# Optimization experiments

Measured on AMD Instinct MI355X. Metric: run time of the kernel, lower is better.

Reference implementation:

```python
import jax, jax.numpy as jnp
import numpy as np

N_HEADS = 16
D_HEAD = 64
D_MODEL = 1024
WINDOW = 256
B, T = 4, 2048


def rotate_half(x):
    x1, x2 = jnp.split(x, 2, axis=-1)
    return jnp.concatenate([-x2, x1], axis=-1)


def apply_rope(x, cos, sin):
    return x * cos + rotate_half(x) * sin


def setup_inputs() -> dict:
    key = jax.random.key(0)
    ks = jax.random.split(key, 5)
    x = jax.random.normal(ks[0], (B, T, D_MODEL), dtype=jnp.float32)
    cos = jax.random.normal(ks[1], (1, T, 1, D_HEAD), dtype=jnp.float32)
    sin = jax.random.normal(ks[2], (1, T, 1, D_HEAD), dtype=jnp.float32)
    qkv_w = jax.random.normal(ks[3], (3 * D_MODEL, D_MODEL), dtype=jnp.float32) * (D_MODEL ** -0.5)
    out_w = jax.random.normal(ks[4], (D_MODEL, D_MODEL), dtype=jnp.float32) * (D_MODEL ** -0.5)
    return {"x": x, "cos": cos, "sin": sin, "qkv_w": qkv_w, "out_w": out_w}


def reference(x, cos, sin, qkv_w, out_w):
    Bc, Tc, C = x.shape
    # QKV projection (bias-free Linear: y = x @ W^T)
    qkv = jnp.einsum('btc,fc->btf', x, qkv_w)
    q, k, v = jnp.split(qkv, 3, axis=-1)
    # [B, H, T, d]
    def to_heads(t):
        return t.reshape(Bc, Tc, N_HEADS, D_HEAD).transpose(0, 2, 1, 3)
    q, k, v = to_heads(q), to_heads(k), to_heads(v)
    # RoPE: cos/sin [1, T, 1, d] -> [1, 1, T, d] broadcasting over heads
    cos_t = cos[:, :Tc].transpose(0, 2, 1, 3)
    sin_t = sin[:, :Tc].transpose(0, 2, 1, 3)
    q = apply_rope(q, cos_t, sin_t)
    k = apply_rope(k, cos_t, sin_t)
    # banded causal mask: allow j <= i and j >= i - (window-1)
    i = jnp.arange(Tc)[:, None]
    j = jnp.arange(Tc)[None, :]
    allowed = (j <= i) & (j >= i - (WINDOW - 1))  # [T, T]
    scale = 1.0 / jnp.sqrt(jnp.asarray(D_HEAD, dtype=q.dtype))
    scores = jnp.einsum('bhqd,bhkd->bhqk', q, k) * scale
    scores = jnp.where(allowed[None, None], scores, jnp.finfo(scores.dtype).min)
    attn = jax.nn.softmax(scores, axis=-1)
    out = jnp.einsum('bhqk,bhkd->bhqd', attn, v)
    out = out.transpose(0, 2, 1, 3).reshape(Bc, Tc, C)
    return jnp.einsum('btc,oc->bto', out, out_w)
```

## Files before the change

kernel.cpp:

```cpp
#include <hip/hip_runtime.h>

typedef __bf16 bf16_t;
typedef __bf16 bf16x8 __attribute__((ext_vector_type(8)));
typedef __bf16 bf16x4 __attribute__((ext_vector_type(4)));
typedef float f32x4 __attribute__((ext_vector_type(4)));

#define GLOAD_LDS16(gptr, lptr)                                                              \
  __builtin_amdgcn_global_load_lds((const __attribute__((address_space(1))) void*)(gptr),    \
                                   (__attribute__((address_space(3))) void*)(lptr), 16, 0, 0)

__device__ __forceinline__ f32x4 f32x4_zero() {
  f32x4 v; v[0] = 0.f; v[1] = 0.f; v[2] = 0.f; v[3] = 0.f; return v;
}

__global__ void cast3_kernel(const float* __restrict__ a, const float* __restrict__ b,
                             const float* __restrict__ c, bf16_t* __restrict__ oa,
                             bf16_t* __restrict__ ob, bf16_t* __restrict__ oc) {
  int i = blockIdx.x * blockDim.x + threadIdx.x;
  const float* src; bf16_t* dst; int j;
  if (i < 2097152) { src = a; dst = oa; j = i; }
  else if (i < 2883584) { src = b; dst = ob; j = i - 2097152; }
  else { src = c; dst = oc; j = i - 2883584; }
  float4 v = ((const float4*)src)[j];
  bf16x4 o;
  o[0] = (bf16_t)v.x; o[1] = (bf16_t)v.y; o[2] = (bf16_t)v.z; o[3] = (bf16_t)v.w;
  ((bf16x4*)dst)[j] = o;
}

template <int MODE>
__global__ __launch_bounds__(256) void gemm_bt_kernel(
    const bf16_t* __restrict__ A, const bf16_t* __restrict__ B, float* __restrict__ C,
    bf16_t* __restrict__ oq, bf16_t* __restrict__ ok_, bf16_t* __restrict__ ov,
    int M, int N, int K) {
  constexpr int BM = 128, BN = 128, BK = 32;
  __shared__ bf16_t As[BM * BK];
  __shared__ bf16_t Bs[BN * BK];
  const int tid = threadIdx.x;
  const int lane = tid & 63;
  const int wid = tid >> 6;
  const int wm = (wid >> 1) * 64;
  const int wn = (wid & 1) * 64;
  const int l16 = lane & 15;
  const int qd = lane >> 4;
  const int bm = blockIdx.x, bn = blockIdx.y;

  const int srow = tid >> 2;
  const int skol = (tid & 3) * 8;

  const bf16_t* gA = A + (size_t)(bm * BM + srow) * K + skol;
  const bf16_t* gB = B + (size_t)(bn * BN + srow) * K + skol;
  bf16_t* lA = &As[srow * BK + skol];
  bf16_t* lB = &Bs[srow * BK + skol];

  f32x4 acc[4][4];
#pragma unroll
  for (int mb = 0; mb < 4; mb++)
#pragma unroll
    for (int nb = 0; nb < 4; nb++) acc[mb][nb] = f32x4_zero();

  for (int k0 = 0; k0 < K; k0 += BK) {
    __syncthreads();
    GLOAD_LDS16(gA + k0, lA);
    GLOAD_LDS16(gA + (size_t)64 * K + k0, lA + 64 * BK);
    GLOAD_LDS16(gB + k0, lB);
    GLOAD_LDS16(gB + (size_t)64 * K + k0, lB + 64 * BK);
    __syncthreads();

    bf16x8 af[4], bfr[4];
#pragma unroll
    for (int mb = 0; mb < 4; mb++)
      af[mb] = *(const bf16x8*)&As[(wm + mb * 16 + l16) * BK + qd * 8];
#pragma unroll
    for (int nb = 0; nb < 4; nb++)
      bfr[nb] = *(const bf16x8*)&Bs[(wn + nb * 16 + l16) * BK + qd * 8];
#pragma unroll
    for (int mb = 0; mb < 4; mb++)
#pragma unroll
      for (int nb = 0; nb < 4; nb++)
        acc[mb][nb] = __builtin_amdgcn_mfma_f32_16x16x32_bf16(af[mb], bfr[nb], acc[mb][nb], 0, 0, 0);
  }

  if (MODE == 0) {
#pragma unroll
    for (int mb = 0; mb < 4; mb++)
#pragma unroll
      for (int nb = 0; nb < 4; nb++)
#pragma unroll
        for (int r = 0; r < 4; r++) {
          int row = bm * BM + wm + mb * 16 + qd * 4 + r;
          int col = bn * BN + wn + nb * 16 + l16;
          C[(size_t)row * N + col] = acc[mb][nb][r];
        }
  } else {
    const int part = bn >> 3;
    const int h = ((bn * 128 + wn) & 1023) >> 6;
    bf16_t* dst = (part == 0) ? oq : (part == 1) ? ok_ : ov;
#pragma unroll
    for (int mb = 0; mb < 4; mb++)
#pragma unroll
      for (int r = 0; r < 4; r++) {
        int row = bm * BM + wm + mb * 16 + qd * 4 + r;
        int b = row >> 11, t = row & 2047;
        size_t basei = (((size_t)(b * 16 + h)) * 2048 + t) * 64;
#pragma unroll
        for (int nb = 0; nb < 4; nb++)
          dst[basei + nb * 16 + l16] = (bf16_t)acc[mb][nb][r];
      }
  }
}

__device__ __forceinline__ void rope_tile_lds(bf16_t* buf, const float* __restrict__ cosp,
                                              const float* __restrict__ sinp, int tbase,
                                              int tid, float sc) {
#pragma unroll
  for (int p2 = 0; p2 < 2; p2++) {
    int it = p2 * 256 + tid;
    int r = it >> 3, pq = it & 7;
    int d0 = pq * 4;
    int t = tbase + r;
    int a_lo = (r * 8 + ((d0 >> 3) ^ (r & 7))) * 8 + (d0 & 7);
    int a_hi = (r * 8 + (((d0 + 32) >> 3) ^ (r & 7))) * 8 + (d0 & 7);
    bf16x4 xl = *(bf16x4*)&buf[a_lo];
    bf16x4 xh = *(bf16x4*)&buf[a_hi];
    float4 cl = *(const float4*)&cosp[t * 64 + d0];
    float4 ch = *(const float4*)&cosp[t * 64 + d0 + 32];
    float4 sl = *(const float4*)&sinp[t * 64 + d0];
    float4 sh = *(const float4*)&sinp[t * 64 + d0 + 32];
    bf16x4 ol, oh;
    ol[0] = (bf16_t)(((float)xl[0] * cl.x - (float)xh[0] * sl.x) * sc);
    ol[1] = (bf16_t)(((float)xl[1] * cl.y - (float)xh[1] * sl.y) * sc);
    ol[2] = (bf16_t)(((float)xl[2] * cl.z - (float)xh[2] * sl.z) * sc);
    ol[3] = (bf16_t)(((float)xl[3] * cl.w - (float)xh[3] * sl.w) * sc);
    oh[0] = (bf16_t)(((float)xh[0] * ch.x + (float)xl[0] * sh.x) * sc);
    oh[1] = (bf16_t)(((float)xh[1] * ch.y + (float)xl[1] * sh.y) * sc);
    oh[2] = (bf16_t)(((float)xh[2] * ch.z + (float)xl[2] * sh.z) * sc);
    oh[3] = (bf16_t)(((float)xh[3] * ch.w + (float)xl[3] * sh.w) * sc);
    *(bf16x4*)&buf[a_lo] = ol;
    *(bf16x4*)&buf[a_hi] = oh;
  }
}

__global__ __launch_bounds__(256) void attn_kernel(
    const bf16_t* __restrict__ qh, const bf16_t* __restrict__ kh,
    const bf16_t* __restrict__ vh, bf16_t* __restrict__ ao,
    const float* __restrict__ cosp, const float* __restrict__ sinp) {
  __shared__ bf16_t qs[64 * 64];
  __shared__ bf16_t ks[64 * 64];
  __shared__ bf16_t vs[64 * 64];
  __shared__ bf16_t vswz[8 * 64 * 8];
  __shared__ bf16_t ps[4][16 * 64];

  const int tid = threadIdx.x;
  const int lane = tid & 63;
  const int wid = tid >> 6;
  const int l16 = lane & 15;
  const int qd = lane >> 4;

  const int bh = blockIdx.x;
  const int i0 = blockIdx.y * 64;
  const int b = bh >> 4, h = bh & 15;

  auto swz4 = [](int f) { int r = f >> 3; return r * 8 + ((f & 7) ^ (r & 7)); };

  {
    const uint4* src = (const uint4*)(qh + ((size_t)bh * 2048 + i0) * 64);
    uint4* dst = (uint4*)qs;
    dst[swz4(tid)] = src[tid];
    dst[swz4(tid + 256)] = src[tid + 256];
  }
  __syncthreads();
  rope_tile_lds(qs, cosp, sinp, i0, tid, 0.18033688011112042f);

  float m_i[4], l_i[4];
  f32x4 oacc[4];
#pragma unroll
  for (int r = 0; r < 4; r++) { m_i[r] = -1e30f; l_i[r] = 0.f; }
#pragma unroll
  for (int nb = 0; nb < 4; nb++) oacc[nb] = f32x4_zero();

  const int c1 = i0 >> 6;
  const int c0 = (c1 >= 4) ? (c1 - 4) : 0;

  for (int c = c0; c <= c1; c++) {
    const int j0 = c * 64;
    __syncthreads();
    {
      const uint4* ksrc = (const uint4*)(kh + ((size_t)bh * 2048 + j0) * 64);
      const uint4* vsrc = (const uint4*)(vh + ((size_t)bh * 2048 + j0) * 64);
      uint4* kdst = (uint4*)ks; uint4* vdst = (uint4*)vs;
      kdst[swz4(tid)] = ksrc[tid]; kdst[swz4(tid + 256)] = ksrc[tid + 256];
      vdst[tid] = vsrc[tid];       vdst[tid + 256] = vsrc[tid + 256];
    }
    __syncthreads();
    rope_tile_lds(ks, cosp, sinp, j0, tid, 1.0f);
    __syncthreads();

    f32x4 sacc[4];
#pragma unroll
    for (int nb = 0; nb < 4; nb++) sacc[nb] = f32x4_zero();
#pragma unroll
    for (int kk = 0; kk < 2; kk++) {
      bf16x8 afr = *(const bf16x8*)&qs[(wid * 16 + l16) * 64 + (((kk * 4 + qd) ^ (l16 & 7)) * 8)];
#pragma unroll
      for (int nb = 0; nb < 4; nb++) {
        bf16x8 bfr = *(const bf16x8*)&ks[(nb * 16 + l16) * 64 + (((kk * 4 + qd) ^ (l16 & 7)) * 8)];
        sacc[nb] = __builtin_amdgcn_mfma_f32_16x16x32_bf16(afr, bfr, sacc[nb], 0, 0, 0);
      }
    }

#pragma unroll
    for (int p2 = 0; p2 < 2; p2++) {
      int F = p2 * 256 + tid;
      int lfrag = F & 63;
      int combo = F >> 6;
      int jbase = (combo >> 2) * 32 + (lfrag >> 4) * 8;
      int d = (combo & 3) * 16 + (lfrag & 15);
      bf16x8 v8;
#pragma unroll
      for (int e = 0; e < 8; e++) v8[e] = vs[(jbase + e) * 64 + d];
      *(bf16x8*)&vswz[(combo * 64 + lfrag) * 8] = v8;
    }

    float rmax[4];
#pragma unroll
    for (int r = 0; r < 4; r++) {
      const int i = i0 + wid * 16 + qd * 4 + r;
#pragma unroll
      for (int nb = 0; nb < 4; nb++) {
        const int j = j0 + nb * 16 + l16;
        bool valid = (j <= i) && (j + 256 > i);
        if (!valid) sacc[nb][r] = -1e30f;
      }
      float rm = fmaxf(fmaxf(sacc[0][r], sacc[1][r]), fmaxf(sacc[2][r], sacc[3][r]));
#pragma unroll
      for (int off = 8; off >= 1; off >>= 1) rm = fmaxf(rm, __shfl_xor(rm, off));
      rmax[r] = rm;
    }

#pragma unroll
    for (int r = 0; r < 4; r++) {
      float mnew = fmaxf(m_i[r], rmax[r]);
      float alpha = exp2f(m_i[r] - mnew);
      m_i[r] = mnew;
      float rowsum = 0.f;
      const int i = i0 + wid * 16 + qd * 4 + r;
      const int prow = qd * 4 + r;
#pragma unroll
      for (int nb = 0; nb < 4; nb++) {
        const int j = j0 + nb * 16 + l16;
        bool valid = (j <= i) && (j + 256 > i);
        float p = valid ? exp2f(sacc[nb][r] - mnew) : 0.f;
        rowsum += p;
        ps[wid][prow * 64 + (((nb * 2 + (l16 >> 3)) ^ (prow & 7)) * 8) + (l16 & 7)] = (bf16_t)p;
      }
#pragma unroll
      for (int off = 8; off >= 1; off >>= 1) rowsum += __shfl_xor(rowsum, off);
      l_i[r] = l_i[r] * alpha + rowsum;
#pragma unroll
      for (int nb = 0; nb < 4; nb++) oacc[nb][r] *= alpha;
    }

    __syncthreads();

#pragma unroll
    for (int kk = 0; kk < 2; kk++) {
      bf16x8 afr = *(const bf16x8*)&ps[wid][l16 * 64 + (((kk * 4 + qd) ^ (l16 & 7)) * 8)];
#pragma unroll
      for (int nb = 0; nb < 4; nb++) {
        bf16x8 bfr = *(const bf16x8*)&vswz[((kk * 4 + nb) * 64 + lane) * 8];
        oacc[nb] = __builtin_amdgcn_mfma_f32_16x16x32_bf16(afr, bfr, oacc[nb], 0, 0, 0);
      }
    }
  }

#pragma unroll
  for (int nb = 0; nb < 4; nb++) {
#pragma unroll
    for (int r = 0; r < 4; r++) {
      int t = i0 + wid * 16 + qd * 4 + r;
      ao[((size_t)(b * 2048 + t)) * 1024 + h * 64 + nb * 16 + l16] =
          (bf16_t)(oacc[nb][r] / l_i[r]);
    }
  }
}

extern "C" void kernel_launch(void* const* d_in, const int* in_sizes, int n_in,
                              void* d_out, int out_size, void* d_ws, size_t ws_size,
                              hipStream_t stream) {
  const float* x    = (const float*)d_in[0];
  const float* cosp = (const float*)d_in[1];
  const float* sinp = (const float*)d_in[2];
  const float* qkvw = (const float*)d_in[3];
  const float* outw = (const float*)d_in[4];
  float* out = (float*)d_out;

  char* ws = (char*)d_ws;
  bf16_t* xb  = (bf16_t*)(ws + 0);
  bf16_t* qwb = (bf16_t*)(ws + 16777216);
  bf16_t* owb = (bf16_t*)(ws + 23068672);
  bf16_t* qhp = (bf16_t*)(ws + 25165824);
  bf16_t* khp = (bf16_t*)(ws + 41943040);
  bf16_t* vhp = (bf16_t*)(ws + 58720256);
  bf16_t* aop = (bf16_t*)(ws + 75497472);

  cast3_kernel<<<12288, 256, 0, stream>>>(x, qkvw, outw, xb, qwb, owb);

  gemm_bt_kernel<1><<<dim3(64, 24), 256, 0, stream>>>(xb, qwb, nullptr, qhp, khp, vhp,
                                                      8192, 3072, 1024);
  attn_kernel<<<dim3(64, 32), 256, 0, stream>>>(qhp, khp, vhp, aop, cosp, sinp);
  gemm_bt_kernel<0><<<dim3(64, 8), 256, 0, stream>>>(aop, owb, out, nullptr, nullptr, nullptr,
                                                     8192, 1024, 1024);
}
```

Baseline: 248.9 us.

## Prefetch K/V tiles into registers and apply RoPE in registers before LDS store

```diff
diff --git a/kernel.cpp b/kernel.cpp
--- a/kernel.cpp
+++ b/kernel.cpp
@@ -12,6 +12,8 @@
 __device__ __forceinline__ f32x4 f32x4_zero() {
   f32x4 v; v[0] = 0.f; v[1] = 0.f; v[2] = 0.f; v[3] = 0.f; return v;
 }
+
+__device__ __forceinline__ int kxr(int r) { return (r & 7) ^ (((r >> 3) & 3) << 1); }
 
 __global__ void cast3_kernel(const float* __restrict__ a, const float* __restrict__ b,
                              const float* __restrict__ c, bf16_t* __restrict__ oa,
@@ -109,35 +111,27 @@
   }
 }
 
-__device__ __forceinline__ void rope_tile_lds(bf16_t* buf, const float* __restrict__ cosp,
-                                              const float* __restrict__ sinp, int tbase,
-                                              int tid, float sc) {
-#pragma unroll
-  for (int p2 = 0; p2 < 2; p2++) {
-    int it = p2 * 256 + tid;
-    int r = it >> 3, pq = it & 7;
-    int d0 = pq * 4;
-    int t = tbase + r;
-    int a_lo = (r * 8 + ((d0 >> 3) ^ (r & 7))) * 8 + (d0 & 7);
-    int a_hi = (r * 8 + (((d0 + 32) >> 3) ^ (r & 7))) * 8 + (d0 & 7);
-    bf16x4 xl = *(bf16x4*)&buf[a_lo];
-    bf16x4 xh = *(bf16x4*)&buf[a_hi];
-    float4 cl = *(const float4*)&cosp[t * 64 + d0];
-    float4 ch = *(const float4*)&cosp[t * 64 + d0 + 32];
-    float4 sl = *(const float4*)&sinp[t * 64 + d0];
-    float4 sh = *(const float4*)&sinp[t * 64 + d0 + 32];
-    bf16x4 ol, oh;
-    ol[0] = (bf16_t)(((float)xl[0] * cl.x - (float)xh[0] * sl.x) * sc);
-    ol[1] = (bf16_t)(((float)xl[1] * cl.y - (float)xh[1] * sl.y) * sc);
-    ol[2] = (bf16_t)(((float)xl[2] * cl.z - (float)xh[2] * sl.z) * sc);
-    ol[3] = (bf16_t)(((float)xl[3] * cl.w - (float)xh[3] * sl.w) * sc);
-    oh[0] = (bf16_t)(((float)xh[0] * ch.x + (float)xl[0] * sh.x) * sc);
-    oh[1] = (bf16_t)(((float)xh[1] * ch.y + (float)xl[1] * sh.y) * sc);
-    oh[2] = (bf16_t)(((float)xh[2] * ch.z + (float)xl[2] * sh.z) * sc);
-    oh[3] = (bf16_t)(((float)xh[3] * ch.w + (float)xl[3] * sh.w) * sc);
-    *(bf16x4*)&buf[a_lo] = ol;
-    *(bf16x4*)&buf[a_hi] = oh;
-  }
+__device__ __forceinline__ bf16x8 rope8(uint4 x, int qq, int t, float sc,
+                                        const float* __restrict__ cosp,
+                                        const float* __restrict__ sinp) {
+  uint4 p;
+  p.x = __shfl_xor((int)x.x, 4); p.y = __shfl_xor((int)x.y, 4);
+  p.z = __shfl_xor((int)x.z, 4); p.w = __shfl_xor((int)x.w, 4);
+  bf16x8 xv = __builtin_bit_cast(bf16x8, x);
+  bf16x8 pv = __builtin_bit_cast(bf16x8, p);
+  const int d0 = qq * 8;
+  const float sgn = (qq < 4) ? -1.f : 1.f;
+  float4 cA = *(const float4*)&cosp[t * 64 + d0];
+  float4 cB = *(const float4*)&cosp[t * 64 + d0 + 4];
+  float4 sA = *(const float4*)&sinp[t * 64 + d0];
+  float4 sB = *(const float4*)&sinp[t * 64 + d0 + 4];
+  float cc[8] = {cA.x, cA.y, cA.z, cA.w, cB.x, cB.y, cB.z, cB.w};
+  float ss[8] = {sA.x, sA.y, sA.z, sA.w, sB.x, sB.y, sB.z, sB.w};
+  bf16x8 o;
+#pragma unroll
+  for (int e = 0; e < 8; e++)
+    o[e] = (bf16_t)(((float)xv[e] * cc[e] + sgn * (float)pv[e] * ss[e]) * sc);
+  return o;
 }
 
 __global__ __launch_bounds__(256) void attn_kernel(
@@ -160,16 +154,34 @@
   const int i0 = blockIdx.y * 64;
   const int b = bh >> 4, h = bh & 15;
 
-  auto swz4 = [](int f) { int r = f >> 3; return r * 8 + ((f & 7) ^ (r & 7)); };
-
-  {
-    const uint4* src = (const uint4*)(qh + ((size_t)bh * 2048 + i0) * 64);
-    uint4* dst = (uint4*)qs;
-    dst[swz4(tid)] = src[tid];
-    dst[swz4(tid + 256)] = src[tid + 256];
-  }
-  __syncthreads();
-  rope_tile_lds(qs, cosp, sinp, i0, tid, 0.18033688011112042f);
+  const int r0 = tid >> 3;
+  const int q0 = tid & 7;
+
+  const uint4* qsrc = (const uint4*)(qh + ((size_t)bh * 2048 + i0) * 64);
+  const uint4* ksrc = (const uint4*)(kh + (size_t)bh * 2048 * 64);
+  const uint4* vsrc = (const uint4*)(vh + (size_t)bh * 2048 * 64);
+
+  const int c1 = i0 >> 6;
+  const int c0 = (c1 >= 4) ? (c1 - 4) : 0;
+
+  uint4 qr0 = qsrc[tid], qr1 = qsrc[tid + 256];
+  uint4 kr0 = ksrc[c0 * 512 + tid], kr1 = ksrc[c0 * 512 + tid + 256];
+  uint4 vr0 = vsrc[c0 * 512 + tid], vr1 = vsrc[c0 * 512 + tid + 256];
+
+  uint4* qs4 = (uint4*)qs;
+  uint4* ks4 = (uint4*)ks;
+  uint4* vs4 = (uint4*)vs;
+
+  *(bf16x8*)&qs4[r0 * 8 + (q0 ^ kxr(r0))] =
+      rope8(qr0, q0, i0 + r0, 0.18033688011112042f, cosp, sinp);
+  *(bf16x8*)&qs4[(r0 + 32) * 8 + (q0 ^ kxr(r0 + 32))] =
+      rope8(qr1, q0, i0 + r0 + 32, 0.18033688011112042f, cosp, sinp);
+  vs4[r0 * 8 + (q0 ^ kxr(r0))] = vr0;
+  vs4[(r0 + 32) * 8 + (q0 ^ kxr(r0 + 32))] = vr1;
+  *(bf16x8*)&ks4[r0 * 8 + (q0 ^ kxr(r0))] =
+      rope8(kr0, q0, c0 * 64 + r0, 1.0f, cosp, sinp);
+  *(bf16x8*)&ks4[(r0 + 32) * 8 + (q0 ^ kxr(r0 + 32))] =
+      rope8(kr1, q0, c0 * 64 + r0 + 32, 1.0f, cosp, sinp);
 
   float m_i[4], l_i[4];
   f32x4 oacc[4];
@@ -178,47 +190,38 @@
 #pragma unroll
   for (int nb = 0; nb < 4; nb++) oacc[nb] = f32x4_zero();
 
-  const int c1 = i0 >> 6;
-  const int c0 = (c1 >= 4) ? (c1 - 4) : 0;
-
-  for (int c = c0; c <= c1; c++) {
+  for (int c = c0;; c++) {
     const int j0 = c * 64;
     __syncthreads();
-    {
-      const uint4* ksrc = (const uint4*)(kh + ((size_t)bh * 2048 + j0) * 64);
-      const uint4* vsrc = (const uint4*)(vh + ((size_t)bh * 2048 + j0) * 64);
-      uint4* kdst = (uint4*)ks; uint4* vdst = (uint4*)vs;
-      kdst[swz4(tid)] = ksrc[tid]; kdst[swz4(tid + 256)] = ksrc[tid + 256];
-      vdst[tid] = vsrc[tid];       vdst[tid + 256] = vsrc[tid + 256];
-    }
-    __syncthreads();
-    rope_tile_lds(ks, cosp, sinp, j0, tid, 1.0f);
-    __syncthreads();
 
     f32x4 sacc[4];
 #pragma unroll
     for (int nb = 0; nb < 4; nb++) sacc[nb] = f32x4_zero();
 #pragma unroll
     for (int kk = 0; kk < 2; kk++) {
-      bf16x8 afr = *(const bf16x8*)&qs[(wid * 16 + l16) * 64 + (((kk * 4 + qd) ^ (l16 & 7)) * 8)];
+      const int arow = wid * 16 + l16;
+      bf16x8 afr = *(const bf16x8*)&qs[arow * 64 + (((kk * 4 + qd) ^ kxr(arow)) * 8)];
 #pragma unroll
       for (int nb = 0; nb < 4; nb++) {
-        bf16x8 bfr = *(const bf16x8*)&ks[(nb * 16 + l16) * 64 + (((kk * 4 + qd) ^ (l16 & 7)) * 8)];
+        const int brow = nb * 16 + l16;
+        bf16x8 bfr = *(const bf16x8*)&ks[brow * 64 + (((kk * 4 + qd) ^ kxr(brow)) * 8)];
         sacc[nb] = __builtin_amdgcn_mfma_f32_16x16x32_bf16(afr, bfr, sacc[nb], 0, 0, 0);
       }
     }
 
 #pragma unroll
     for (int p2 = 0; p2 < 2; p2++) {
-      int F = p2 * 256 + tid;
-      int lfrag = F & 63;
-      int combo = F >> 6;
-      int jbase = (combo >> 2) * 32 + (lfrag >> 4) * 8;
-      int d = (combo & 3) * 16 + (lfrag & 15);
+      int combo = p2 * 4 + wid;
+      int jbase = (combo >> 2) * 32 + (lane >> 4) * 8;
+      int dcol = (combo & 3) * 16 + (lane & 15);
+      int bb = dcol >> 3, dlo = dcol & 7;
       bf16x8 v8;
 #pragma unroll
-      for (int e = 0; e < 8; e++) v8[e] = vs[(jbase + e) * 64 + d];
-      *(bf16x8*)&vswz[(combo * 64 + lfrag) * 8] = v8;
+      for (int e = 0; e < 8; e++) {
+        int row = jbase + e;
+        v8[e] = vs[row * 64 + ((bb ^ kxr(row)) * 8) + dlo];
+      }
+      *(bf16x8*)&vswz[(combo * 64 + lane) * 8] = v8;
     }
 
     float rmax[4];
@@ -251,7 +254,7 @@
         bool valid = (j <= i) && (j + 256 > i);
         float p = valid ? exp2f(sacc[nb][r] - mnew) : 0.f;
         rowsum += p;
-        ps[wid][prow * 64 + (((nb * 2 + (l16 >> 3)) ^ (prow & 7)) * 8) + (l16 & 7)] = (bf16_t)p;
+        ps[wid][prow * 64 + (((nb * 2 + (l16 >> 3)) ^ kxr(prow)) * 8) + (l16 & 7)] = (bf16_t)p;
       }
 #pragma unroll
       for (int off = 8; off >= 1; off >>= 1) rowsum += __shfl_xor(rowsum, off);
@@ -262,15 +265,29 @@
 
     __syncthreads();
 
+    const bool more = (c < c1);
+    if (more) {
+      kr0 = ksrc[(c + 1) * 512 + tid]; kr1 = ksrc[(c + 1) * 512 + tid + 256];
+      vr0 = vsrc[(c + 1) * 512 + tid]; vr1 = vsrc[(c + 1) * 512 + tid + 256];
+    }
+
 #pragma unroll
     for (int kk = 0; kk < 2; kk++) {
-      bf16x8 afr = *(const bf16x8*)&ps[wid][l16 * 64 + (((kk * 4 + qd) ^ (l16 & 7)) * 8)];
+      bf16x8 afr = *(const bf16x8*)&ps[wid][l16 * 64 + (((kk * 4 + qd) ^ kxr(l16)) * 8)];
 #pragma unroll
       for (int nb = 0; nb < 4; nb++) {
         bf16x8 bfr = *(const bf16x8*)&vswz[((kk * 4 + nb) * 64 + lane) * 8];
         oacc[nb] = __builtin_amdgcn_mfma_f32_16x16x32_bf16(afr, bfr, oacc[nb], 0, 0, 0);
       }
     }
+
+    if (!more) break;
+    vs4[r0 * 8 + (q0 ^ kxr(r0))] = vr0;
+    vs4[(r0 + 32) * 8 + (q0 ^ kxr(r0 + 32))] = vr1;
+    *(bf16x8*)&ks4[r0 * 8 + (q0 ^ kxr(r0))] =
+        rope8(kr0, q0, (c + 1) * 64 + r0, 1.0f, cosp, sinp);
+    *(bf16x8*)&ks4[(r0 + 32) * 8 + (q0 ^ kxr(r0 + 32))] =
+        rope8(kr1, q0, (c + 1) * 64 + r0 + 32, 1.0f, cosp, sinp);
   }
 
 #pragma unroll
```

New measurement: 258.0 us. 1.04x slower.
